# Kernel tuning notes

Measured on AMD Instinct MI355X. Metric: run time of the kernel, lower is better.

Reference implementation:

```python
import jax, jax.numpy as jnp
import numpy as np

N, C, D = 2048, 1000, 768
KNN = 5          # module default
SIGMA = 1.0      # unused by kNN affinity (matches original kNN_affinity)
BOUND_LAMBDA = 1.0
MAX_STEPS = 100


def setup_inputs() -> dict:
    key = jax.random.key(0)
    k1, k2 = jax.random.split(key)
    logits = jax.random.normal(k1, (N, C), dtype=jnp.float32) * 2.0
    feats = jax.random.normal(k2, (N, D), dtype=jnp.float32)
    return {"logits": logits, "feats": feats}


def _knn_affinity(feats, knn):
    # feats are L2-normalized, so squared euclidean dist = 2 - 2 * <xi, xj>
    n = feats.shape[0]
    sim = feats @ feats.T                                  # [N, N]
    dist = jnp.sqrt(jnp.clip(2.0 - 2.0 * sim, 0.0))        # [N, N]
    _, idx = jax.lax.top_k(-dist, knn + 1)                 # knn+1 smallest distances
    idx = idx[:, 1:]                                       # drop self (dist 0)
    W = jnp.zeros((n, n), dtype=feats.dtype)
    W = W.at[jnp.arange(n)[:, None], idx].set(1.0)
    return W


def _entropy_energy(Y, unary, pairwise, lam):
    return jnp.sum(unary * Y - lam * pairwise * Y + Y * jnp.log(jnp.clip(Y, 1e-20)))


def _laplacian_optimization(unary, kernel, lam=BOUND_LAMBDA, max_steps=MAX_STEPS):
    Y0 = jax.nn.softmax(-unary, axis=-1)

    def cond(state):
        _, _, i, done = state
        return (i < max_steps) & jnp.logical_not(done)

    def body(state):
        Y, oldE, i, _ = state
        pairwise = lam * (kernel @ Y)                      # [N, C]
        Ynew = jax.nn.softmax(pairwise - unary, axis=-1)
        E = _entropy_energy(Ynew, unary, pairwise, lam)
        done = (i > 1) & (jnp.abs(E - oldE) <= 1e-8 * jnp.abs(oldE))
        return (Ynew, E, i + 1, done)

    Y, _, _, _ = jax.lax.while_loop(
        cond, body, (Y0, jnp.float32(jnp.inf), jnp.int32(0), jnp.array(False))
    )
    return Y


def reference(logits, feats):
    probas = jax.nn.softmax(logits, axis=1)
    unary = -jnp.log(probas + 1e-10)                       # [N, C]
    f = feats / jnp.linalg.norm(feats, axis=-1, keepdims=True)
    kernel = _knn_affinity(f, KNN)                         # [N, N] binary
    kernel = 0.5 * (kernel + kernel.T)                     # force_symmetry=True
    return _laplacian_optimization(unary, kernel)
```

## Files before the change

### kernel.cpp

```cpp
#include <hip/hip_runtime.h>
#include <hip/hip_cooperative_groups.h>
#include <math.h>

namespace cg = cooperative_groups;

#define N_ 2048
#define C_ 1000
#define D_ 768
#define K_ 5
#define CAP_ 128
#define MAXS_ 100
#define LB_ 128
#define LT_ 512

typedef unsigned short ushort_t;
typedef unsigned int uint_t;

__device__ inline float bflo(uint_t v) { union { uint_t i; float f; } c; c.i = v << 16; return c.f; }
__device__ inline float bfhi(uint_t v) { union { uint_t i; float f; } c; c.i = v & 0xffff0000u; return c.f; }
__device__ inline ushort_t f2b(float f) {
    union { float f; uint_t i; } c; c.f = f;
    return (ushort_t)((c.i + 0x7fffu + ((c.i >> 16) & 1u)) >> 16);
}
__device__ inline uint_t pk(float a, float b) { return (uint_t)f2b(a) | ((uint_t)f2b(b) << 16); }

__global__ __launch_bounds__(256) void k_norm(const float* __restrict__ feats,
                                              float* __restrict__ fn) {
    const int r = blockIdx.x, tid = threadIdx.x;
    __shared__ float red[256];
    const float* row = feats + (size_t)r * D_;
    float ss = 0.f;
    for (int c = tid; c < D_; c += 256) { float v = row[c]; ss += v * v; }
    red[tid] = ss; __syncthreads();
    for (int s = 128; s > 0; s >>= 1) { if (tid < s) red[tid] += red[tid + s]; __syncthreads(); }
    const float n = sqrtf(red[0]); __syncthreads();
    for (int c = tid; c < D_; c += 256) fn[(size_t)r * D_ + c] = row[c] / n;
}

#define GTM 128
#define GTN 128
#define GBK 32
__global__ __launch_bounds__(512, 2) void k_gemm(const float* __restrict__ A,
                                                 float* __restrict__ Csim) {
    __shared__ float As[GBK][GTM + 4];
    __shared__ float Bs[GBK][GTN + 4];
    const int tid = threadIdx.x;
    const int tx = tid & 31;
    const int ty = tid >> 5;
    const int m0 = blockIdx.y * GTM, n0 = blockIdx.x * GTN;
    float acc[8][4] = {};
    for (int k0 = 0; k0 < D_; k0 += GBK) {
        #pragma unroll
        for (int l = 0; l < 2; l++) {
            int idx = tid + l * 512;
            int mm = idx >> 3, kk = (idx & 7) * 4;
            float4 v = *(const float4*)(A + (size_t)(m0 + mm) * D_ + k0 + kk);
            As[kk][mm] = v.x; As[kk + 1][mm] = v.y; As[kk + 2][mm] = v.z; As[kk + 3][mm] = v.w;
        }
        #pragma unroll
        for (int l = 0; l < 2; l++) {
            int idx = tid + l * 512;
            int mm = idx >> 3, kk = (idx & 7) * 4;
            float4 v = *(const float4*)(A + (size_t)(n0 + mm) * D_ + k0 + kk);
            Bs[kk][mm] = v.x; Bs[kk + 1][mm] = v.y; Bs[kk + 2][mm] = v.z; Bs[kk + 3][mm] = v.w;
        }
        __syncthreads();
        #pragma unroll
        for (int kk = 0; kk < GBK; kk++) {
            float4 a0 = *(const float4*)&As[kk][ty * 8];
            float4 a1 = *(const float4*)&As[kk][ty * 8 + 4];
            float4 bv = *(const float4*)&Bs[kk][tx * 4];
            float a[8] = { a0.x, a0.y, a0.z, a0.w, a1.x, a1.y, a1.z, a1.w };
            float b[4] = { bv.x, bv.y, bv.z, bv.w };
            #pragma unroll
            for (int i = 0; i < 8; i++)
                #pragma unroll
                for (int j = 0; j < 4; j++) acc[i][j] += a[i] * b[j];
        }
        __syncthreads();
    }
    #pragma unroll
    for (int i = 0; i < 8; i++) {
        float4 st = make_float4(acc[i][0], acc[i][1], acc[i][2], acc[i][3]);
        *(float4*)(Csim + (size_t)(m0 + ty * 8 + i) * N_ + n0 + tx * 4) = st;
    }
}

__global__ __launch_bounds__(256) void k_topk(const float* __restrict__ sim,
                                              int* __restrict__ knn,
                                              int* __restrict__ indeg,
                                              int* __restrict__ inlist) {
    const int r = blockIdx.x, tid = threadIdx.x;
    float bd[6]; int bi[6];
    #pragma unroll
    for (int k = 0; k < 6; k++) { bd[k] = INFINITY; bi[k] = 0x7fffffff; }
    const float* srow = sim + (size_t)r * N_;
    for (int j = tid; j < N_; j += 256) {
        float s = srow[j];
        float d = sqrtf(fmaxf(2.f - 2.f * s, 0.f));
        if (d < bd[5] || (d == bd[5] && j < bi[5])) {
            int k = 5;
            while (k > 0 && (d < bd[k - 1] || (d == bd[k - 1] && j < bi[k - 1]))) {
                bd[k] = bd[k - 1]; bi[k] = bi[k - 1]; k--;
            }
            bd[k] = d; bi[k] = j;
        }
    }
    __shared__ float sd[256][6];
    __shared__ int   si[256][6];
    #pragma unroll
    for (int k = 0; k < 6; k++) { sd[tid][k] = bd[k]; si[tid][k] = bi[k]; }
    __syncthreads();
    for (int s = 128; s > 0; s >>= 1) {
        if (tid < s) {
            float md[6]; int mi[6];
            int p = 0, q = 0;
            #pragma unroll
            for (int k = 0; k < 6; k++) {
                float d1 = sd[tid][p], d2 = sd[tid + s][q];
                int i1 = si[tid][p], i2 = si[tid + s][q];
                bool take1 = (d1 < d2) || (d1 == d2 && i1 < i2);
                if (take1) { md[k] = d1; mi[k] = i1; p++; } else { md[k] = d2; mi[k] = i2; q++; }
            }
            #pragma unroll
            for (int k = 0; k < 6; k++) { sd[tid][k] = md[k]; si[tid][k] = mi[k]; }
        }
        __syncthreads();
    }
    if (tid < K_) {
        const int j = si[0][1 + tid];
        knn[(size_t)r * K_ + tid] = j;
        const int pos = atomicAdd(&indeg[j], 1);
        if (pos < CAP_) inlist[(size_t)j * CAP_ + pos] = r;
    }
}

__global__ __launch_bounds__(LT_) void k_lame(
    const float* __restrict__ logits, const int* __restrict__ knn,
    const int* __restrict__ indeg, const int* __restrict__ inlist,
    ushort_t* __restrict__ YA, ushort_t* __restrict__ YB,
    float* __restrict__ partials, int* __restrict__ flag,
    float* __restrict__ out)
{
    cg::grid_group grid = cg::this_grid();
    const int tid = threadIdx.x;
    const int wave = tid >> 6, lane = tid & 63;
    const int rbase = blockIdx.x * 16 + wave * 2;
    const int c0 = lane * 16;
    const bool msk0 = lane <= 62;
    const bool msk1 = lane <= 61;

    __shared__ int nb[16][K_ + CAP_ + 3];
    __shared__ int cnts[16];
    #pragma unroll
    for (int rr = 0; rr < 2; rr++) {
        const int w = wave * 2 + rr, r = rbase + rr;
        if (lane == 0) cnts[w] = K_ + min(indeg[r], CAP_);
        if (lane < K_) nb[w][lane] = knn[r * K_ + lane];
        for (int t = lane; t < CAP_; t += 64) nb[w][K_ + t] = inlist[(size_t)r * CAP_ + t];
    }
    __syncthreads();
    if (lane < 2) {
        const int w = wave * 2 + lane;
        int* L = &nb[w][K_];
        const int cn = cnts[w] - K_;
        for (int a = 1; a < cn; a++) {
            const int key = L[a];
            int b = a - 1;
            while (b >= 0 && L[b] > key) { L[b + 1] = L[b]; b--; }
            L[b + 1] = key;
        }
    }
    __syncthreads();
    const int cnt2[2] = { cnts[wave * 2], cnts[wave * 2 + 1] };

    float u[2][16];
    #pragma unroll
    for (int rr = 0; rr < 2; rr++) {
        const float* lp = logits + (size_t)(rbase + rr) * C_;
        float l[16];
        #pragma unroll
        for (int q = 0; q < 4; q++) {
            const int off = c0 + q * 4;
            const int ao = (off + 3 < C_) ? off : 0;
            float4 v = *(const float4*)(lp + ao);
            l[q * 4 + 0] = v.x; l[q * 4 + 1] = v.y; l[q * 4 + 2] = v.z; l[q * 4 + 3] = v.w;
        }
        float mm = -INFINITY;
        #pragma unroll
        for (int k = 0; k < 8; k++) mm = fmaxf(mm, msk0 ? l[k] : -INFINITY);
        #pragma unroll
        for (int k = 8; k < 16; k++) mm = fmaxf(mm, msk1 ? l[k] : -INFINITY);
        #pragma unroll
        for (int o = 32; o > 0; o >>= 1) mm = fmaxf(mm, __shfl_xor(mm, o));
        float e[16];
        float s = 0.f;
        #pragma unroll
        for (int k = 0; k < 8; k++) { e[k] = msk0 ? expf(l[k] - mm) : 0.f; s += e[k]; }
        #pragma unroll
        for (int k = 8; k < 16; k++) { e[k] = msk1 ? expf(l[k] - mm) : 0.f; s += e[k]; }
        #pragma unroll
        for (int o = 32; o > 0; o >>= 1) s += __shfl_xor(s, o);
        const float inv = 1.f / s;
        #pragma unroll
        for (int k = 0; k < 16; k++) u[rr][k] = -logf(e[k] * inv + 1e-10f);
    }

    auto gather = [&](const ushort_t* __restrict__ src, int rr, float* acc) {
        const int w = wave * 2 + rr, cn = cnt2[rr];
        auto acc16 = [&](uint4 p, uint4 q) {
            acc[0] += bflo(p.x); acc[1] += bfhi(p.x); acc[2] += bflo(p.y); acc[3] += bfhi(p.y);
            acc[4] += bflo(p.z); acc[5] += bfhi(p.z); acc[6] += bflo(p.w); acc[7] += bfhi(p.w);
            acc[8] += bflo(q.x); acc[9] += bfhi(q.x); acc[10] += bflo(q.y); acc[11] += bfhi(q.y);
            acc[12] += bflo(q.z); acc[13] += bfhi(q.z); acc[14] += bflo(q.w); acc[15] += bfhi(q.w);
        };
        int t = 0;
        for (; t + 2 <= cn; t += 2) {
            const int n0 = nb[w][t], n1 = nb[w][t + 1];
            const uint4 p0 = *(const uint4*)(src + (size_t)n0 * C_ + c0);
            const uint4 p1 = *(const uint4*)(src + (size_t)n0 * C_ + c0 + 8);
            const uint4 q0 = *(const uint4*)(src + (size_t)n1 * C_ + c0);
            const uint4 q1 = *(const uint4*)(src + (size_t)n1 * C_ + c0 + 8);
            acc16(p0, p1); acc16(q0, q1);
        }
        if (t < cn) {
            const int n0 = nb[w][t];
            const uint4 p0 = *(const uint4*)(src + (size_t)n0 * C_ + c0);
            const uint4 p1 = *(const uint4*)(src + (size_t)n0 * C_ + c0 + 8);
            acc16(p0, p1);
        }
    };

    auto smax = [&](int rr, const float* acc, ushort_t* __restrict__ dst) -> float {
        const int r = rbase + rr;
        float z[16];
        #pragma unroll
        for (int k = 0; k < 16; k++) z[k] = 0.5f * acc[k] - u[rr][k];
        float mm = -INFINITY;
        #pragma unroll
        for (int k = 0; k < 8; k++) mm = fmaxf(mm, msk0 ? z[k] : -INFINITY);
        #pragma unroll
        for (int k = 8; k < 16; k++) mm = fmaxf(mm, msk1 ? z[k] : -INFINITY);
        #pragma unroll
        for (int o = 32; o > 0; o >>= 1) mm = fmaxf(mm, __shfl_xor(mm, o));
        float e[16];
        float s = 0.f;
        #pragma unroll
        for (int k = 0; k < 8; k++) { e[k] = msk0 ? expf(z[k] - mm) : 0.f; s += e[k]; }
        #pragma unroll
        for (int k = 8; k < 16; k++) { e[k] = msk1 ? expf(z[k] - mm) : 0.f; s += e[k]; }
        #pragma unroll
        for (int o = 32; o > 0; o >>= 1) s += __shfl_xor(s, o);
        const float inv = 1.f / s;
        if (msk0) {
            uint4 w;
            w.x = pk(e[0] * inv, e[1] * inv); w.y = pk(e[2] * inv, e[3] * inv);
            w.z = pk(e[4] * inv, e[5] * inv); w.w = pk(e[6] * inv, e[7] * inv);
            *(uint4*)(dst + (size_t)r * C_ + c0) = w;
        }
        if (msk1) {
            uint4 w;
            w.x = pk(e[8] * inv, e[9] * inv); w.y = pk(e[10] * inv, e[11] * inv);
            w.z = pk(e[12] * inv, e[13] * inv); w.w = pk(e[14] * inv, e[15] * inv);
            *(uint4*)(dst + (size_t)r * C_ + c0 + 8) = w;
        }
        return -(mm + logf(s));
    };

    {
        float zacc[16];
        #pragma unroll
        for (int k = 0; k < 16; k++) zacc[k] = 0.f;
        smax(0, zacc, YA);
        smax(1, zacc, YA);
    }
    if (blockIdx.x == 0 && tid == 0) { flag[0] = 0; flag[1] = 0; }
    grid.sync();

    float oldE = INFINITY;
    const ushort_t* fin = YB;
    for (int it = 0; it < MAXS_; ++it) {
        const ushort_t* src = (it & 1) ? YB : YA;
        ushort_t* dst = (it & 1) ? YA : YB;
        float acc0[16], acc1[16];
        #pragma unroll
        for (int k = 0; k < 16; k++) { acc0[k] = 0.f; acc1[k] = 0.f; }
        gather(src, 0, acc0);
        gather(src, 1, acc1);
        const float E0 = smax(0, acc0, dst);
        const float E1 = smax(1, acc1, dst);
        if (lane == 0) {
            partials[(size_t)(it & 1) * N_ + rbase] = E0;
            partials[(size_t)(it & 1) * N_ + rbase + 1] = E1;
        }
        grid.sync();
        if (blockIdx.x == 0 && wave == 0) {
            const float* P = partials + (size_t)(it & 1) * N_;
            float e = 0.f;
            #pragma unroll
            for (int q = 0; q < 32; q += 4) {
                float4 v = *(const float4*)(P + lane * 32 + q);
                e += ((v.x + v.y) + v.z) + v.w;
            }
            #pragma unroll
            for (int o = 32; o > 0; o >>= 1) e += __shfl_xor(e, o);
            const bool done = (it > 1) && (fabsf(e - oldE) <= 1e-8f * fabsf(oldE));
            oldE = e;
            if (lane == 0) flag[it & 1] = done ? 1 : 0;
        }
        fin = dst;
        if (((volatile const int*)flag)[(it + 1) & 1]) break;
    }

    #pragma unroll
    for (int rr = 0; rr < 2; rr++) {
        const int r = rbase + rr;
        #pragma unroll
        for (int q = 0; q < 4; q++) {
            if (c0 + q * 4 + 3 < C_) {
                const uint2 w = *(const uint2*)(fin + (size_t)r * C_ + c0 + q * 4);
                float4 o;
                o.x = bflo(w.x); o.y = bfhi(w.x); o.z = bflo(w.y); o.w = bfhi(w.y);
                *(float4*)(out + (size_t)r * C_ + c0 + q * 4) = o;
            }
        }
    }
}

extern "C" void kernel_launch(void* const* d_in, const int* in_sizes, int n_in,
                              void* d_out, int out_size, void* d_ws, size_t ws_size,
                              hipStream_t stream) {
    const float* logits = (const float*)d_in[0];
    const float* feats  = (const float*)d_in[1];
    float* out = (float*)d_out;
    char* ws = (char*)d_ws;

    size_t off = 0;
    auto alloc = [&](size_t b) { size_t o = off; off += (b + 255) & ~(size_t)255; return o; };
    float* fn      = (float*)(ws + alloc((size_t)N_ * D_ * 4));
    float* sim     = (float*)(ws + alloc((size_t)N_ * N_ * 4));
    int*   knn     = (int*)(ws + alloc((size_t)N_ * K_ * 4));
    int*   indeg   = (int*)(ws + alloc((size_t)N_ * 4));
    int*   inlist  = (int*)(ws + alloc((size_t)N_ * CAP_ * 4));
    float* partials= (float*)(ws + alloc((size_t)2 * N_ * 4));
    int*   flag    = (int*)(ws + alloc(256));
    if (off > ws_size) return;

    ushort_t* YA = (ushort_t*)sim;
    ushort_t* YB = YA + (size_t)N_ * C_;

    k_norm <<<N_, 256, 0, stream>>>(feats, fn);
    (void)hipMemsetAsync(indeg, 0, (size_t)N_ * 4, stream);
    k_gemm <<<dim3(N_ / GTN, N_ / GTM), 512, 0, stream>>>(fn, sim);
    k_topk <<<N_, 256, 0, stream>>>(sim, knn, indeg, inlist);

    const float* p_logits = logits;
    const int* p_knn = knn;
    const int* p_indeg = indeg;
    const int* p_inlist = inlist;
    ushort_t* p_YA = YA;
    ushort_t* p_YB = YB;
    float* p_part = partials;
    int* p_flag = flag;
    float* p_out = out;
    void* args[] = { &p_logits, &p_knn, &p_indeg, &p_inlist, &p_YA, &p_YB, &p_part, &p_flag, &p_out };
    (void)hipLaunchCooperativeKernel((void*)k_lame, dim3(LB_), dim3(LT_), args, 0, stream);
}
```

Before: 358.8 us.

## Use one wave per row in top-k and defer flag check past gather

The top-k kernel now assigns one 64-lane wave per row and merges the per-lane 6-best lists with xor shuffles. This replaces the 256-thread shared-memory tree reduction and its repeated block barriers. In the Laplacian loop, the convergence flag is read right after the grid sync but only acted on after the next iteration's gather. That moves the volatile flag read off the critical path, at the cost of one extra speculative gather before exiting.

```diff
diff --git a/kernel.cpp b/kernel.cpp
--- a/kernel.cpp
+++ b/kernel.cpp
@@ -90,14 +90,15 @@
                                               int* __restrict__ knn,
                                               int* __restrict__ indeg,
                                               int* __restrict__ inlist) {
-    const int r = blockIdx.x, tid = threadIdx.x;
+    const int wave = threadIdx.x >> 6, lane = threadIdx.x & 63;
+    const int r = blockIdx.x * 4 + wave;
     float bd[6]; int bi[6];
     #pragma unroll
     for (int k = 0; k < 6; k++) { bd[k] = INFINITY; bi[k] = 0x7fffffff; }
     const float* srow = sim + (size_t)r * N_;
-    for (int j = tid; j < N_; j += 256) {
-        float s = srow[j];
-        float d = sqrtf(fmaxf(2.f - 2.f * s, 0.f));
+    for (int j = lane; j < N_; j += 64) {
+        const float s = srow[j];
+        const float d = sqrtf(fmaxf(2.f - 2.f * s, 0.f));
         if (d < bd[5] || (d == bd[5] && j < bi[5])) {
             int k = 5;
             while (k > 0 && (d < bd[k - 1] || (d == bd[k - 1] && j < bi[k - 1]))) {
@@ -106,30 +107,25 @@
             bd[k] = d; bi[k] = j;
         }
     }
-    __shared__ float sd[256][6];
-    __shared__ int   si[256][6];
-    #pragma unroll
-    for (int k = 0; k < 6; k++) { sd[tid][k] = bd[k]; si[tid][k] = bi[k]; }
-    __syncthreads();
-    for (int s = 128; s > 0; s >>= 1) {
-        if (tid < s) {
-            float md[6]; int mi[6];
-            int p = 0, q = 0;
-            #pragma unroll
-            for (int k = 0; k < 6; k++) {
-                float d1 = sd[tid][p], d2 = sd[tid + s][q];
-                int i1 = si[tid][p], i2 = si[tid + s][q];
-                bool take1 = (d1 < d2) || (d1 == d2 && i1 < i2);
-                if (take1) { md[k] = d1; mi[k] = i1; p++; } else { md[k] = d2; mi[k] = i2; q++; }
-            }
-            #pragma unroll
-            for (int k = 0; k < 6; k++) { sd[tid][k] = md[k]; si[tid][k] = mi[k]; }
-        }
-        __syncthreads();
-    }
-    if (tid < K_) {
-        const int j = si[0][1 + tid];
-        knn[(size_t)r * K_ + tid] = j;
+    #pragma unroll
+    for (int o = 1; o <= 32; o <<= 1) {
+        float od[6]; int oj[6];
+        #pragma unroll
+        for (int k = 0; k < 6; k++) { od[k] = __shfl_xor(bd[k], o); oj[k] = __shfl_xor(bi[k], o); }
+        float md[6]; int mi[6];
+        int p = 0, q = 0;
+        #pragma unroll
+        for (int k = 0; k < 6; k++) {
+            const bool take1 = (bd[p] < od[q]) || (bd[p] == od[q] && bi[p] < oj[q]);
+            if (take1) { md[k] = bd[p]; mi[k] = bi[p]; p++; }
+            else       { md[k] = od[q]; mi[k] = oj[q]; q++; }
+        }
+        #pragma unroll
+        for (int k = 0; k < 6; k++) { bd[k] = md[k]; bi[k] = mi[k]; }
+    }
+    if (lane < K_) {
+        const int j = bi[1 + lane];
+        knn[(size_t)r * K_ + lane] = j;
         const int pos = atomicAdd(&indeg[j], 1);
         if (pos < CAP_) inlist[(size_t)j * CAP_ + pos] = r;
     }
@@ -278,6 +274,7 @@
     grid.sync();
 
     float oldE = INFINITY;
+    int flagpref = 0;
     const ushort_t* fin = YB;
     for (int it = 0; it < MAXS_; ++it) {
         const ushort_t* src = (it & 1) ? YB : YA;
@@ -287,6 +284,7 @@
         for (int k = 0; k < 16; k++) { acc0[k] = 0.f; acc1[k] = 0.f; }
         gather(src, 0, acc0);
         gather(src, 1, acc1);
+        if (flagpref) break;
         const float E0 = smax(0, acc0, dst);
         const float E1 = smax(1, acc1, dst);
         if (lane == 0) {
@@ -308,8 +306,8 @@
             oldE = e;
             if (lane == 0) flag[it & 1] = done ? 1 : 0;
         }
+        flagpref = ((volatile const int*)flag)[(it + 1) & 1];
         fin = dst;
-        if (((volatile const int*)flag)[(it + 1) & 1]) break;
     }
 
     #pragma unroll
@@ -352,7 +350,7 @@
     k_norm <<<N_, 256, 0, stream>>>(feats, fn);
     (void)hipMemsetAsync(indeg, 0, (size_t)N_ * 4, stream);
     k_gemm <<<dim3(N_ / GTN, N_ / GTM), 512, 0, stream>>>(fn, sim);
-    k_topk <<<N_, 256, 0, stream>>>(sim, knn, indeg, inlist);
+    k_topk <<<N_ / 4, 256, 0, stream>>>(sim, knn, indeg, inlist);
 
     const float* p_logits = logits;
     const int* p_knn = knn;
```

Measured after the change: 382.2 us. 1.07x slower.
